# Optimization experiments

Hardware: AMD Instinct MI355X
Metric: run time of the kernel (lower is better)

Reference implementation:

```python
import jax, jax.numpy as jnp
import numpy as np

T, U, H, P, UC = 256, 512, 64, 1024, 10000
LAMBDA_T = 0.1      # temporal decay rate (Flashback default scale)
LAMBDA_S = 100.0    # spatial decay rate
DAY = 86400.0


def setup_inputs() -> dict:
    key = jax.random.key(0)
    ks = jax.random.split(key, 12)
    sc = 0.02
    x = jax.random.randint(ks[0], (T, U), 0, P)
    # timestamps, increasing along the sequence axis (checkin order)
    t = jnp.sort(jax.random.uniform(ks[1], (T, U)) * (7.0 * DAY), axis=0)
    t_slot = jax.random.randint(ks[2], (T, U), 0, 168)
    s = jax.random.normal(ks[3], (T, U, 2))
    y = jax.random.randint(ks[4], (T, U), 0, P)
    h = jnp.zeros((U, H), jnp.float32)
    active_user = jax.random.randint(ks[5], (U,), 0, UC)
    poi_emb = jax.random.normal(ks[6], (P, H)) * sc
    user_emb = jax.random.normal(ks[7], (UC, H)) * sc
    Wx = jax.random.normal(ks[8], (H, 3 * H)) * sc
    Wh = jax.random.normal(ks[9], (H, 3 * H)) * sc
    b = jnp.zeros((3 * H,), jnp.float32)
    fc_W = jax.random.normal(ks[10], (2 * H, P)) * sc
    fc_b = jnp.zeros((P,), jnp.float32)
    return dict(x=x, t=t, t_slot=t_slot, s=s, y=y, h=h, active_user=active_user,
                poi_emb=poi_emb, user_emb=user_emb, Wx=Wx, Wh=Wh, b=b,
                fc_W=fc_W, fc_b=fc_b)


def _gru_scan(x_emb, h0, Wx, Wh, b):
    # x_emb: [T,U,H], h0: [U,H]
    def step(hprev, xt):
        gx = xt @ Wx + b          # [U,3H]
        gh = hprev @ Wh           # [U,3H]
        rx, zx, nx = jnp.split(gx, 3, axis=-1)
        rh, zh, nh = jnp.split(gh, 3, axis=-1)
        r = jax.nn.sigmoid(rx + rh)
        z = jax.nn.sigmoid(zx + zh)
        n = jnp.tanh(nx + r * nh)
        hn = (1.0 - z) * hprev + z * n
        return hn, hn
    hT, outs = jax.lax.scan(step, h0, x_emb)
    return outs, hT  # [T,U,H], [U,H]


def reference(x, t, t_slot, s, y, h, active_user,
              poi_emb, user_emb, Wx, Wh, b, fc_W, fc_b):
    seq_len, user_len = x.shape
    x_emb = poi_emb[x]                 # [T,U,H]  (stands in for pre_model emb)
    p_u = user_emb[active_user]        # [U,H]
    out, hT = _gru_scan(x_emb, h, Wx, Wh, b)  # RNN outputs [T,U,H]

    # Pairwise spatiotemporal decay weights, vectorized over (i,j,user).
    dt = t[:, None, :] - t[None, :, :]                    # [T,T,U]
    ds = jnp.linalg.norm(s[:, None, :, :] - s[None, :, :, :], axis=-1)  # [T,T,U]
    f_t = 0.5 * (jnp.cos(dt * (2.0 * jnp.pi / DAY)) + 1.0) * jnp.exp(-(dt / DAY) * LAMBDA_T)
    f_s = jnp.exp(-ds * LAMBDA_S)
    causal = jnp.tril(jnp.ones((seq_len, seq_len), dtype=bool))  # j <= i
    w = jnp.where(causal[:, :, None], f_t * f_s + 1e-10, 0.0)     # [T,T,U]
    sum_w = jnp.sum(w, axis=1)                                    # [T,U]
    out_w = jnp.einsum('iju,juh->iuh', w, out) / sum_w[:, :, None]  # [T,U,H]

    feats = jnp.concatenate(
        [out_w, jnp.broadcast_to(p_u[None], (seq_len, user_len, p_u.shape[-1]))],
        axis=-1)                                                  # [T,U,2H]
    y_linear = feats @ fc_W + fc_b                                # [T,U,P]
    return y_linear, hT
```

## Files before the change

### kernel.cpp

```cpp
#include <hip/hip_runtime.h>

#define T_N 256
#define U_N 512
#define H_N 64
#define P_N 1024

typedef __attribute__((ext_vector_type(8))) short short8;
typedef __attribute__((ext_vector_type(4))) short short4v;
typedef __attribute__((ext_vector_type(4))) unsigned short ushort4v;
typedef __attribute__((ext_vector_type(4))) float f32x4;

#define MFMA __builtin_amdgcn_mfma_f32_16x16x32_bf16

#define LGKM_BARRIER() asm volatile("s_waitcnt lgkmcnt(0)\ns_barrier" ::: "memory")

__device__ __forceinline__ short f2bf(float f) {
  union { float f; unsigned u; } v; v.f = f;
  unsigned r = v.u + 0x7FFFu + ((v.u >> 16) & 1u);
  return (short)(r >> 16);
}

__device__ __forceinline__ unsigned cvtpk(float lo, float hi) {
  unsigned r;
  asm("v_cvt_pk_bf16_f32 %0, %1, %2" : "=v"(r) : "v"(lo), "v"(hi));
  return r;
}

__device__ __forceinline__ short8 pack8(float4 a, float4 b) {
  union { unsigned u[4]; short8 s; } z;
  z.u[0] = cvtpk(a.x, a.y); z.u[1] = cvtpk(a.z, a.w);
  z.u[2] = cvtpk(b.x, b.y); z.u[3] = cvtpk(b.z, b.w);
  return z.s;
}

__device__ __forceinline__ float bfu_lo(unsigned u) {
  union { unsigned x; float f; } v; v.x = u << 16; return v.f;
}
__device__ __forceinline__ float bfu_hi(unsigned u) {
  union { unsigned x; float f; } v; v.x = u & 0xffff0000u; return v.f;
}

__global__ __launch_bounds__(256) void k_pack(
    const float* __restrict__ Wx, const float* __restrict__ Wh,
    const float* __restrict__ fcW, short* __restrict__ wxp,
    short* __restrict__ whp, short* __restrict__ bp) {
  if (blockIdx.x < 12) {
    int idx = blockIdx.x * 256 + threadIdx.x;
    int m = idx / 1536;
    int r = idx % 1536;
    const float* W = m ? Wh : Wx;
    short* op = m ? whp : wxp;
    int ks = r / 768, lk = (r / 192) & 3, g = r % 192;
#pragma unroll
    for (int e = 0; e < 8; ++e)
      op[(size_t)r * 8 + e] = f2bf(W[(ks * 32 + lk * 8 + e) * 192 + g]);
  } else {
    int sidx = (blockIdx.x - 12) * 256 + threadIdx.x;
    int s = sidx & 1023;
    int kg = (sidx >> 10) & 3;
    int ks = sidx >> 12;
    int L = (s & ~63) + 4 * (s & 15) + ((s >> 4) & 3);
#pragma unroll
    for (int e = 0; e < 8; ++e) {
      int k = ks * 32 + kg * 8 + e;
      bp[((size_t)((ks * 4 + kg) * P_N + s)) * 8 + e] = f2bf(fcW[k * P_N + L]);
    }
  }
}

__global__ __launch_bounds__(256) void k_gx(
    const int* __restrict__ x, const float* __restrict__ poi_emb,
    const short* __restrict__ wxp, const float* __restrict__ b,
    char* __restrict__ gxp) {
  int wave = threadIdx.x >> 6, lane = threadIdx.x & 63;
  int lr = lane & 15, lk = lane >> 4;
  int tile = blockIdx.x * 4 + wave;
  int row = tile * 16 + lr;
  int xv = x[row];
  const float* pb = poi_emb + (size_t)xv * H_N + lk * 8;
  float4 v0 = *(const float4*)pb, v1 = *(const float4*)(pb + 4);
  float4 v2 = *(const float4*)(pb + 32), v3 = *(const float4*)(pb + 36);
  short8 ax0 = pack8(v0, v1), ax1 = pack8(v2, v3);
#pragma unroll
  for (int j = 0; j < 12; ++j) {
    float bc = b[16 * j + lr];
    f32x4 acc = {bc, bc, bc, bc};
    short8 bf0 = *(const short8*)&wxp[((size_t)((0 * 4 + lk) * 192 + 16 * j + lr)) * 8];
    short8 bf1 = *(const short8*)&wxp[((size_t)((1 * 4 + lk) * 192 + 16 * j + lr)) * 8];
    acc = MFMA(ax0, bf0, acc, 0, 0, 0);
    acc = MFMA(ax1, bf1, acc, 0, 0, 0);
    uint2 pk;
    pk.x = cvtpk(acc[0], acc[1]);
    pk.y = cvtpk(acc[2], acc[3]);
    *(uint2*)(gxp + (((size_t)tile * 12 + j) * 64 + lane) * 8) = pk;
  }
}

__global__ __launch_bounds__(256) void k_scan2(
    const char* __restrict__ gxp, const float* __restrict__ h0,
    const short* __restrict__ whp, short* __restrict__ out_bf,
    float* __restrict__ hT) {
  int ublk = blockIdx.x;
  int u0 = ublk * 16;
  int tid = threadIdx.x;
  int w = tid >> 6, lane = tid & 63, lr = lane & 15, lk = lane >> 4;
  __shared__ __align__(16) float h_lds[8][16][68];
  int sgr = 16 * w, sgz = 64 + 16 * w, sgn = 128 + 16 * w;
  short8 fhr[2], fhz[2], fhn[2];
#pragma unroll
  for (int ks = 0; ks < 2; ++ks) {
    size_t base = (size_t)((ks * 4 + lk) * 192) * 8;
    fhr[ks] = *(const short8*)&whp[base + (size_t)(sgr + lr) * 8];
    fhz[ks] = *(const short8*)&whp[base + (size_t)(sgz + lr) * 8];
    fhn[ks] = *(const short8*)&whp[base + (size_t)(sgn + lr) * 8];
  }
  for (int idx = tid; idx < 16 * 64; idx += 256)
    h_lds[7][idx >> 6][idx & 63] = h0[(size_t)(u0 + (idx >> 6)) * H_N + (idx & 63)];
  __syncthreads();
  float hp[4];
#pragma unroll
  for (int e = 0; e < 4; ++e) hp[e] = h_lds[7][4 * lk + e][16 * w + lr];
  short8 ah0, ah1;
  {
    float4 q0 = *(float4*)&h_lds[7][lr][8 * lk];
    float4 q1 = *(float4*)&h_lds[7][lr][8 * lk + 4];
    float4 q2 = *(float4*)&h_lds[7][lr][32 + 8 * lk];
    float4 q3 = *(float4*)&h_lds[7][lr][32 + 8 * lk + 4];
    ah0 = pack8(q0, q1); ah1 = pack8(q2, q3);
  }
  const char* gbase = gxp + (((size_t)ublk * 12 + w) * 64 + lane) * 8;
  uint2 pr0, pr1, pr2, pr3, pz0, pz1, pz2, pz3, pn0, pn1, pn2, pn3;
#define PF(sl, tt) { size_t o = (size_t)(tt) * 196608; \
    pr##sl = *(const uint2*)(gbase + o); \
    pz##sl = *(const uint2*)(gbase + o + 2048); \
    pn##sl = *(const uint2*)(gbase + o + 4096); }
  PF(0, 0) PF(1, 1) PF(2, 2) PF(3, 3)
  int fu = tid >> 4, fh = (tid & 15) * 4;
  for (int t8 = 0; t8 < T_N; t8 += 8) {
#define GATE(E, TB) { \
      float r = 1.f / (1.f + __expf(-accr[E])); \
      float z = 1.f / (1.f + __expf(-accz[E])); \
      float npre = accnx[E] + r * accnh[E]; \
      float e2 = __expf(2.f * npre); \
      float n = 1.f - 2.f / (e2 + 1.f); \
      float hn = hp[E] + z * (n - hp[E]); \
      hp[E] = hn; \
      h_lds[TB][4 * lk + E][16 * w + lr] = hn; }
#define BODY(TB, SL) { \
      f32x4 accr = {bfu_lo(pr##SL.x), bfu_hi(pr##SL.x), bfu_lo(pr##SL.y), bfu_hi(pr##SL.y)}; \
      f32x4 accz = {bfu_lo(pz##SL.x), bfu_hi(pz##SL.x), bfu_lo(pz##SL.y), bfu_hi(pz##SL.y)}; \
      f32x4 accnx = {bfu_lo(pn##SL.x), bfu_hi(pn##SL.x), bfu_lo(pn##SL.y), bfu_hi(pn##SL.y)}; \
      f32x4 accnh = {0.f, 0.f, 0.f, 0.f}; \
      int tpf = t8 + TB + 4; if (tpf > 255) tpf = 255; \
      PF(SL, tpf) \
      accr = MFMA(ah0, fhr[0], accr, 0, 0, 0); \
      accr = MFMA(ah1, fhr[1], accr, 0, 0, 0); \
      accz = MFMA(ah0, fhz[0], accz, 0, 0, 0); \
      accz = MFMA(ah1, fhz[1], accz, 0, 0, 0); \
      accnh = MFMA(ah0, fhn[0], accnh, 0, 0, 0); \
      accnh = MFMA(ah1, fhn[1], accnh, 0, 0, 0); \
      GATE(0, TB) GATE(1, TB) GATE(2, TB) GATE(3, TB) \
      LGKM_BARRIER(); \
      { \
        float4 q0 = *(float4*)&h_lds[TB][lr][8 * lk]; \
        float4 q1 = *(float4*)&h_lds[TB][lr][8 * lk + 4]; \
        float4 q2 = *(float4*)&h_lds[TB][lr][32 + 8 * lk]; \
        float4 q3 = *(float4*)&h_lds[TB][lr][32 + 8 * lk + 4]; \
        ah0 = pack8(q0, q1); ah1 = pack8(q2, q3); \
      } }
    BODY(0, 0) BODY(1, 1) BODY(2, 2) BODY(3, 3)
    BODY(4, 0) BODY(5, 1) BODY(6, 2) BODY(7, 3)
#pragma unroll
    for (int s = 0; s < 8; ++s) {
      float4 fv = *(float4*)&h_lds[s][fu][fh];
      uint2 pkd;
      pkd.x = cvtpk(fv.x, fv.y);
      pkd.y = cvtpk(fv.z, fv.w);
      *(uint2*)&out_bf[(size_t)(t8 + s) * (U_N * H_N) + (size_t)u0 * H_N + tid * 4] = pkd;
    }
    LGKM_BARRIER();
  }
  for (int idx = tid; idx < 16 * 64; idx += 256)
    hT[(size_t)(u0 + (idx >> 6)) * H_N + (idx & 63)] = h_lds[7][idx >> 6][idx & 63];
}

__global__ __launch_bounds__(256) void k_ub(
    const int* __restrict__ active_user, const float* __restrict__ user_emb,
    const float* __restrict__ fcW, const float* __restrict__ fcb,
    float* __restrict__ ub) {
  int u = blockIdx.x;
  int tid = threadIdx.x;
  __shared__ float pu[H_N];
  if (tid < H_N) pu[tid] = user_emb[active_user[u] * H_N + tid];
  __syncthreads();
  for (int p = tid; p < P_N; p += 256) {
    float acc = fcb[p];
#pragma unroll
    for (int k = 0; k < H_N; ++k) acc += pu[k] * fcW[(H_N + k) * P_N + p];
    ub[u * P_N + p] = acc;
  }
}

__global__ __launch_bounds__(256) void k_stage2(
    const float* __restrict__ t, const float* __restrict__ s,
    const short* __restrict__ out_bf, short* __restrict__ apk) {
  int u = blockIdx.x;
  int tid = threadIdx.x;
  __shared__ __align__(16) unsigned short outT[H_N][264];
  __shared__ __align__(16) unsigned short wlT[16][264];
  __shared__ float tU[T_N];
  __shared__ float sUx[T_N], sUy[T_N];
  for (int idx = tid; idx < T_N * 8; idx += 256) {
    int jr = idx >> 3, gp = idx & 7;
    short8 v = *(const short8*)&out_bf[((size_t)jr * U_N + u) * H_N + gp * 8];
#pragma unroll
    for (int e = 0; e < 8; ++e) outT[gp * 8 + e][jr] = (unsigned short)v[e];
  }
  {
    int jr = tid;
    tU[jr] = t[jr * U_N + u];
    sUx[jr] = s[((size_t)jr * U_N + u) * 2];
    sUy[jr] = s[((size_t)jr * U_N + u) * 2 + 1];
  }
  __syncthreads();
  int lane = tid & 63, wv = tid >> 6;
  int lr = lane & 15, lk = lane >> 4;
  int j = tid;
  float tj = tU[j], sx = sUx[j], sy = sUy[j];
  short8 ones;
#pragma unroll
  for (int e = 0; e < 8; ++e) ones[e] = (short)0x3F80;
  for (int c = 0; c < 16; ++c) {
#pragma unroll
    for (int iqq = 0; iqq < 16; ++iqq) {
      int i = c * 16 + iqq;
      float wv_ = 0.f;
      if (j <= i) {
        float dt = tU[i] - tj;
        float dx = sUx[i] - sx, dy = sUy[i] - sy;
        float dsn = sqrtf(dx * dx + dy * dy);
        float arg = dt * (-1.1574074074074074e-06f) - 100.0f * dsn;
        float ft = 0.5f * (__cosf(dt * 7.2722052166430395e-05f) + 1.0f);
        wv_ = ft * __expf(arg) + 1e-10f;
      }
      wlT[iqq][j] = (unsigned short)f2bf(wv_);
    }
    __syncthreads();
    f32x4 acc = {0.f, 0.f, 0.f, 0.f};
    f32x4 acc1 = {0.f, 0.f, 0.f, 0.f};
    int nk = (c + 2) >> 1;
    for (int kk = 0; kk < nk; ++kk) {
      short8 aw = *(const short8*)&wlT[lr][kk * 32 + 8 * lk];
      short8 bo = *(const short8*)&outT[16 * wv + lr][kk * 32 + 8 * lk];
      acc = MFMA(aw, bo, acc, 0, 0, 0);
      acc1 = MFMA(aw, ones, acc1, 0, 0, 0);
    }
#pragma unroll
    for (int e = 0; e < 4; ++e) {
      int i = c * 16 + 4 * lk + e;
      float val = acc[e] * (1.f / acc1[e]);
      apk[((size_t)i * U_N + u) * H_N + 16 * wv + lr] = f2bf(val);
    }
    __syncthreads();
  }
}

__global__ __launch_bounds__(256) void k_fc(
    const short* __restrict__ apk, const short* __restrict__ Bp,
    const float* __restrict__ ub, float* __restrict__ C) {
  int s_ = blockIdx.x;
  int xcd = s_ & 7, q = s_ >> 3;
  int bm = xcd * 128 + (q >> 3);
  int bn = q & 7;
  int tid = threadIdx.x;
  int wave = tid >> 6, lane = tid & 63;
  int wm = wave >> 1, wn = wave & 1;
  int row0 = bm * 128 + wm * 64;
  int col0 = bn * 128 + wn * 64;
  int lr = lane & 15, lk = lane >> 4;
  f32x4 acc[4][4] = {};
#pragma unroll
  for (int ks = 0; ks < 2; ++ks) {
    short8 af[4];
#pragma unroll
    for (int m = 0; m < 4; ++m)
      af[m] = *(const short8*)&apk[((size_t)(row0 + m * 16 + lr)) * H_N + ks * 32 + lk * 8];
#pragma unroll
    for (int n = 0; n < 4; ++n) {
      short8 bf = *(const short8*)&Bp[((size_t)((ks * 4 + lk) * P_N + col0 + n * 16 + lr)) * 8];
#pragma unroll
      for (int m = 0; m < 4; ++m)
        acc[m][n] = MFMA(af[m], bf, acc[m][n], 0, 0, 0);
    }
  }
#pragma unroll
  for (int m = 0; m < 4; ++m) {
    int rbase = row0 + m * 16 + lk * 4;
#pragma unroll
    for (int r = 0; r < 4; ++r) {
      int row = rbase + r;
      int uu = row & (U_N - 1);
      f32x4 ubv = *(const f32x4*)&ub[(size_t)uu * P_N + col0 + 4 * lr];
      f32x4 v;
      v[0] = acc[m][0][r] + ubv[0];
      v[1] = acc[m][1][r] + ubv[1];
      v[2] = acc[m][2][r] + ubv[2];
      v[3] = acc[m][3][r] + ubv[3];
      __builtin_nontemporal_store(v, (f32x4*)&C[(size_t)row * P_N + col0 + 4 * lr]);
    }
  }
}

extern "C" void kernel_launch(void* const* d_in, const int* in_sizes, int n_in,
                              void* d_out, int out_size, void* d_ws, size_t ws_size,
                              hipStream_t stream) {
  const int*   x           = (const int*)d_in[0];
  const float* t           = (const float*)d_in[1];
  const float* s           = (const float*)d_in[3];
  const float* h0          = (const float*)d_in[5];
  const int*   active_user = (const int*)d_in[6];
  const float* poi_emb     = (const float*)d_in[7];
  const float* user_emb    = (const float*)d_in[8];
  const float* Wx          = (const float*)d_in[9];
  const float* Wh          = (const float*)d_in[10];
  const float* b           = (const float*)d_in[11];
  const float* fcW         = (const float*)d_in[12];
  const float* fcb         = (const float*)d_in[13];

  float* y_out = (float*)d_out;
  float* hT = y_out + (size_t)T_N * U_N * P_N;

  char* ws = (char*)d_ws;
  short* out_bf = (short*)ws;
  char*  gxp    = ws + 16777216;
  short* apk    = (short*)(ws + 16777216);
  float* ub     = (float*)(ws + 67108864);
  short* bp     = (short*)(ws + 69206016);
  short* wxp    = (short*)(ws + 69337088);
  short* whp    = (short*)(ws + 69361664);

  k_pack<<<44, 256, 0, stream>>>(Wx, Wh, fcW, wxp, whp, bp);
  k_gx<<<2048, 256, 0, stream>>>(x, poi_emb, wxp, b, gxp);
  k_scan2<<<32, 256, 0, stream>>>(gxp, h0, whp, out_bf, hT);
  k_ub<<<U_N, 256, 0, stream>>>(active_user, user_emb, fcW, fcb, ub);
  k_stage2<<<U_N, 256, 0, stream>>>(t, s, out_bf, apk);
  k_fc<<<8192, 256, 0, stream>>>(apk, bp, ub, y_out);
}
```

Baseline: 418.8 us.

## Pack two user groups per 512-thread block in GRU scan kernel

The GRU scan kernel now runs 16 blocks of 512 threads, each holding two independent 16-user groups with separate LDS slices, instead of 32 blocks of 256. The LDS history ring shrinks from 8 to 4 timesteps per group, so output flushes happen every 4 steps. Barriers now synchronize both groups together, coupling their latency chains, and fewer blocks are spread across CUs; the intent is presumably to let the two groups' MFMA and gate work interleave on one CU.

```diff
diff --git a/kernel.cpp b/kernel.cpp
--- a/kernel.cpp
+++ b/kernel.cpp
@@ -96,15 +96,18 @@
   }
 }
 
-__global__ __launch_bounds__(256) void k_scan2(
+__global__ __launch_bounds__(512) void k_scan2(
     const char* __restrict__ gxp, const float* __restrict__ h0,
     const short* __restrict__ whp, short* __restrict__ out_bf,
     float* __restrict__ hT) {
-  int ublk = blockIdx.x;
-  int u0 = ublk * 16;
   int tid = threadIdx.x;
-  int w = tid >> 6, lane = tid & 63, lr = lane & 15, lk = lane >> 4;
-  __shared__ __align__(16) float h_lds[8][16][68];
+  int g = tid >> 8;
+  int tidg = tid & 255;
+  int w = (tid >> 6) & 3;
+  int lane = tid & 63, lr = lane & 15, lk = lane >> 4;
+  int u0 = blockIdx.x * 32 + g * 16;
+  int ublk = blockIdx.x * 2 + g;
+  __shared__ __align__(16) float h_lds[2][4][16][68];
   int sgr = 16 * w, sgz = 64 + 16 * w, sgn = 128 + 16 * w;
   short8 fhr[2], fhz[2], fhn[2];
 #pragma unroll
@@ -114,18 +117,18 @@
     fhz[ks] = *(const short8*)&whp[base + (size_t)(sgz + lr) * 8];
     fhn[ks] = *(const short8*)&whp[base + (size_t)(sgn + lr) * 8];
   }
-  for (int idx = tid; idx < 16 * 64; idx += 256)
-    h_lds[7][idx >> 6][idx & 63] = h0[(size_t)(u0 + (idx >> 6)) * H_N + (idx & 63)];
+  for (int idx = tidg; idx < 16 * 64; idx += 256)
+    h_lds[g][3][idx >> 6][idx & 63] = h0[(size_t)(u0 + (idx >> 6)) * H_N + (idx & 63)];
   __syncthreads();
   float hp[4];
 #pragma unroll
-  for (int e = 0; e < 4; ++e) hp[e] = h_lds[7][4 * lk + e][16 * w + lr];
+  for (int e = 0; e < 4; ++e) hp[e] = h_lds[g][3][4 * lk + e][16 * w + lr];
   short8 ah0, ah1;
   {
-    float4 q0 = *(float4*)&h_lds[7][lr][8 * lk];
-    float4 q1 = *(float4*)&h_lds[7][lr][8 * lk + 4];
-    float4 q2 = *(float4*)&h_lds[7][lr][32 + 8 * lk];
-    float4 q3 = *(float4*)&h_lds[7][lr][32 + 8 * lk + 4];
+    float4 q0 = *(float4*)&h_lds[g][3][lr][8 * lk];
+    float4 q1 = *(float4*)&h_lds[g][3][lr][8 * lk + 4];
+    float4 q2 = *(float4*)&h_lds[g][3][lr][32 + 8 * lk];
+    float4 q3 = *(float4*)&h_lds[g][3][lr][32 + 8 * lk + 4];
     ah0 = pack8(q0, q1); ah1 = pack8(q2, q3);
   }
   const char* gbase = gxp + (((size_t)ublk * 12 + w) * 64 + lane) * 8;
@@ -135,8 +138,8 @@
     pz##sl = *(const uint2*)(gbase + o + 2048); \
     pn##sl = *(const uint2*)(gbase + o + 4096); }
   PF(0, 0) PF(1, 1) PF(2, 2) PF(3, 3)
-  int fu = tid >> 4, fh = (tid & 15) * 4;
-  for (int t8 = 0; t8 < T_N; t8 += 8) {
+  int fu = tidg >> 4, fh = (tidg & 15) * 4;
+  for (int t4 = 0; t4 < T_N; t4 += 4) {
 #define GATE(E, TB) { \
       float r = 1.f / (1.f + __expf(-accr[E])); \
       float z = 1.f / (1.f + __expf(-accz[E])); \
@@ -145,13 +148,13 @@
       float n = 1.f - 2.f / (e2 + 1.f); \
       float hn = hp[E] + z * (n - hp[E]); \
       hp[E] = hn; \
-      h_lds[TB][4 * lk + E][16 * w + lr] = hn; }
+      h_lds[g][TB][4 * lk + E][16 * w + lr] = hn; }
 #define BODY(TB, SL) { \
       f32x4 accr = {bfu_lo(pr##SL.x), bfu_hi(pr##SL.x), bfu_lo(pr##SL.y), bfu_hi(pr##SL.y)}; \
       f32x4 accz = {bfu_lo(pz##SL.x), bfu_hi(pz##SL.x), bfu_lo(pz##SL.y), bfu_hi(pz##SL.y)}; \
       f32x4 accnx = {bfu_lo(pn##SL.x), bfu_hi(pn##SL.x), bfu_lo(pn##SL.y), bfu_hi(pn##SL.y)}; \
       f32x4 accnh = {0.f, 0.f, 0.f, 0.f}; \
-      int tpf = t8 + TB + 4; if (tpf > 255) tpf = 255; \
+      int tpf = t4 + TB + 4; if (tpf > 255) tpf = 255; \
       PF(SL, tpf) \
       accr = MFMA(ah0, fhr[0], accr, 0, 0, 0); \
       accr = MFMA(ah1, fhr[1], accr, 0, 0, 0); \
@@ -162,26 +165,25 @@
       GATE(0, TB) GATE(1, TB) GATE(2, TB) GATE(3, TB) \
       LGKM_BARRIER(); \
       { \
-        float4 q0 = *(float4*)&h_lds[TB][lr][8 * lk]; \
-        float4 q1 = *(float4*)&h_lds[TB][lr][8 * lk + 4]; \
-        float4 q2 = *(float4*)&h_lds[TB][lr][32 + 8 * lk]; \
-        float4 q3 = *(float4*)&h_lds[TB][lr][32 + 8 * lk + 4]; \
+        float4 q0 = *(float4*)&h_lds[g][TB][lr][8 * lk]; \
+        float4 q1 = *(float4*)&h_lds[g][TB][lr][8 * lk + 4]; \
+        float4 q2 = *(float4*)&h_lds[g][TB][lr][32 + 8 * lk]; \
+        float4 q3 = *(float4*)&h_lds[g][TB][lr][32 + 8 * lk + 4]; \
         ah0 = pack8(q0, q1); ah1 = pack8(q2, q3); \
       } }
     BODY(0, 0) BODY(1, 1) BODY(2, 2) BODY(3, 3)
-    BODY(4, 0) BODY(5, 1) BODY(6, 2) BODY(7, 3)
-#pragma unroll
-    for (int s = 0; s < 8; ++s) {
-      float4 fv = *(float4*)&h_lds[s][fu][fh];
+#pragma unroll
+    for (int s = 0; s < 4; ++s) {
+      float4 fv = *(float4*)&h_lds[g][s][fu][fh];
       uint2 pkd;
       pkd.x = cvtpk(fv.x, fv.y);
       pkd.y = cvtpk(fv.z, fv.w);
-      *(uint2*)&out_bf[(size_t)(t8 + s) * (U_N * H_N) + (size_t)u0 * H_N + tid * 4] = pkd;
+      *(uint2*)&out_bf[(size_t)(t4 + s) * (U_N * H_N) + (size_t)u0 * H_N + tidg * 4] = pkd;
     }
     LGKM_BARRIER();
   }
-  for (int idx = tid; idx < 16 * 64; idx += 256)
-    hT[(size_t)(u0 + (idx >> 6)) * H_N + (idx & 63)] = h_lds[7][idx >> 6][idx & 63];
+  for (int idx = tidg; idx < 16 * 64; idx += 256)
+    hT[(size_t)(u0 + (idx >> 6)) * H_N + (idx & 63)] = h_lds[g][3][idx >> 6][idx & 63];
 }
 
 __global__ __launch_bounds__(256) void k_ub(
@@ -341,7 +343,7 @@
 
   k_pack<<<44, 256, 0, stream>>>(Wx, Wh, fcW, wxp, whp, bp);
   k_gx<<<2048, 256, 0, stream>>>(x, poi_emb, wxp, b, gxp);
-  k_scan2<<<32, 256, 0, stream>>>(gxp, h0, whp, out_bf, hT);
+  k_scan2<<<16, 512, 0, stream>>>(gxp, h0, whp, out_bf, hT);
   k_ub<<<U_N, 256, 0, stream>>>(active_user, user_emb, fcW, fcb, ub);
   k_stage2<<<U_N, 256, 0, stream>>>(t, s, out_bf, apk);
   k_fc<<<8192, 256, 0, stream>>>(apk, bp, ub, y_out);
```

After: 500.6 us. 19.5% more time.

## Write GRU outputs in MFMA-ready transposed layout and drop LDS transpose in stage2

Applied to the files above, without the earlier changes.

The scan kernel now stores its bf16 hidden outputs per user in a [u][t/8][h][8] layout that matches the MFMA B-operand fragment. Stage2 can then read B fragments straight from global memory instead of staging and transposing them through a 33KB LDS buffer. Removing that buffer lets stage2 declare 4 blocks per CU in its launch bounds. The fc kernel also drops its XCD-aware block swizzle in favour of a plain 2D grid, which may hurt L2 locality. The scan store pattern changes to scalar LDS reads with 16-byte global writes.

```diff
diff --git a/kernel.cpp b/kernel.cpp
--- a/kernel.cpp
+++ b/kernel.cpp
@@ -7,7 +7,6 @@
 
 typedef __attribute__((ext_vector_type(8))) short short8;
 typedef __attribute__((ext_vector_type(4))) short short4v;
-typedef __attribute__((ext_vector_type(4))) unsigned short ushort4v;
 typedef __attribute__((ext_vector_type(4))) float f32x4;
 
 #define MFMA __builtin_amdgcn_mfma_f32_16x16x32_bf16
@@ -98,7 +97,7 @@
 
 __global__ __launch_bounds__(256) void k_scan2(
     const char* __restrict__ gxp, const float* __restrict__ h0,
-    const short* __restrict__ whp, short* __restrict__ out_bf,
+    const short* __restrict__ whp, short* __restrict__ out_tr,
     float* __restrict__ hT) {
   int ublk = blockIdx.x;
   int u0 = ublk * 16;
@@ -135,7 +134,6 @@
     pz##sl = *(const uint2*)(gbase + o + 2048); \
     pn##sl = *(const uint2*)(gbase + o + 4096); }
   PF(0, 0) PF(1, 1) PF(2, 2) PF(3, 3)
-  int fu = tid >> 4, fh = (tid & 15) * 4;
   for (int t8 = 0; t8 < T_N; t8 += 8) {
 #define GATE(E, TB) { \
       float r = 1.f / (1.f + __expf(-accr[E])); \
@@ -170,13 +168,19 @@
       } }
     BODY(0, 0) BODY(1, 1) BODY(2, 2) BODY(3, 3)
     BODY(4, 0) BODY(5, 1) BODY(6, 2) BODY(7, 3)
-#pragma unroll
-    for (int s = 0; s < 8; ++s) {
-      float4 fv = *(float4*)&h_lds[s][fu][fh];
-      uint2 pkd;
-      pkd.x = cvtpk(fv.x, fv.y);
-      pkd.y = cvtpk(fv.z, fv.w);
-      *(uint2*)&out_bf[(size_t)(t8 + s) * (U_N * H_N) + (size_t)u0 * H_N + tid * 4] = pkd;
+    {
+      int tb = t8 >> 3;
+#pragma unroll
+      for (int pp = 0; pp < 4; ++pp) {
+        int p = pp * 256 + tid;
+        int uu = p >> 6, hh = p & 63;
+        uint4 pkd;
+        pkd.x = cvtpk(h_lds[0][uu][hh], h_lds[1][uu][hh]);
+        pkd.y = cvtpk(h_lds[2][uu][hh], h_lds[3][uu][hh]);
+        pkd.z = cvtpk(h_lds[4][uu][hh], h_lds[5][uu][hh]);
+        pkd.w = cvtpk(h_lds[6][uu][hh], h_lds[7][uu][hh]);
+        *(uint4*)&out_tr[((((size_t)(u0 + uu)) * 32 + tb) * 64 + hh) * 8] = pkd;
+      }
     }
     LGKM_BARRIER();
   }
@@ -201,21 +205,14 @@
   }
 }
 
-__global__ __launch_bounds__(256) void k_stage2(
+__global__ __launch_bounds__(256, 4) void k_stage2(
     const float* __restrict__ t, const float* __restrict__ s,
-    const short* __restrict__ out_bf, short* __restrict__ apk) {
+    const short* __restrict__ out_tr, short* __restrict__ apk) {
   int u = blockIdx.x;
   int tid = threadIdx.x;
-  __shared__ __align__(16) unsigned short outT[H_N][264];
   __shared__ __align__(16) unsigned short wlT[16][264];
   __shared__ float tU[T_N];
   __shared__ float sUx[T_N], sUy[T_N];
-  for (int idx = tid; idx < T_N * 8; idx += 256) {
-    int jr = idx >> 3, gp = idx & 7;
-    short8 v = *(const short8*)&out_bf[((size_t)jr * U_N + u) * H_N + gp * 8];
-#pragma unroll
-    for (int e = 0; e < 8; ++e) outT[gp * 8 + e][jr] = (unsigned short)v[e];
-  }
   {
     int jr = tid;
     tU[jr] = t[jr * U_N + u];
@@ -227,6 +224,7 @@
   int lr = lane & 15, lk = lane >> 4;
   int j = tid;
   float tj = tU[j], sx = sUx[j], sy = sUy[j];
+  const short* obase = out_tr + (size_t)u * 32 * 64 * 8;
   short8 ones;
 #pragma unroll
   for (int e = 0; e < 8; ++e) ones[e] = (short)0x3F80;
@@ -251,7 +249,7 @@
     int nk = (c + 2) >> 1;
     for (int kk = 0; kk < nk; ++kk) {
       short8 aw = *(const short8*)&wlT[lr][kk * 32 + 8 * lk];
-      short8 bo = *(const short8*)&outT[16 * wv + lr][kk * 32 + 8 * lk];
+      short8 bo = *(const short8*)&obase[(((kk * 4 + lk) * 64) + 16 * wv + lr) * 8];
       acc = MFMA(aw, bo, acc, 0, 0, 0);
       acc1 = MFMA(aw, ones, acc1, 0, 0, 0);
     }
@@ -268,10 +266,7 @@
 __global__ __launch_bounds__(256) void k_fc(
     const short* __restrict__ apk, const short* __restrict__ Bp,
     const float* __restrict__ ub, float* __restrict__ C) {
-  int s_ = blockIdx.x;
-  int xcd = s_ & 7, q = s_ >> 3;
-  int bm = xcd * 128 + (q >> 3);
-  int bn = q & 7;
+  int bm = blockIdx.y, bn = blockIdx.x;
   int tid = threadIdx.x;
   int wave = tid >> 6, lane = tid & 63;
   int wm = wave >> 1, wn = wave & 1;
@@ -331,7 +326,7 @@
   float* hT = y_out + (size_t)T_N * U_N * P_N;
 
   char* ws = (char*)d_ws;
-  short* out_bf = (short*)ws;
+  short* out_tr = (short*)ws;
   char*  gxp    = ws + 16777216;
   short* apk    = (short*)(ws + 16777216);
   float* ub     = (float*)(ws + 67108864);
@@ -341,8 +336,8 @@
 
   k_pack<<<44, 256, 0, stream>>>(Wx, Wh, fcW, wxp, whp, bp);
   k_gx<<<2048, 256, 0, stream>>>(x, poi_emb, wxp, b, gxp);
-  k_scan2<<<32, 256, 0, stream>>>(gxp, h0, whp, out_bf, hT);
+  k_scan2<<<32, 256, 0, stream>>>(gxp, h0, whp, out_tr, hT);
   k_ub<<<U_N, 256, 0, stream>>>(active_user, user_emb, fcW, fcb, ub);
-  k_stage2<<<U_N, 256, 0, stream>>>(t, s, out_bf, apk);
-  k_fc<<<8192, 256, 0, stream>>>(apk, bp, ub, y_out);
-}
+  k_stage2<<<U_N, 256, 0, stream>>>(t, s, out_tr, apk);
+  k_fc<<<dim3(8, 1024), 256, 0, stream>>>(apk, bp, ub, y_out);
+}
```

Result: no change. 418.0 us (-0.2%).
